# Kernel tuning notes

Measured on AMD Instinct MI355X. Metric: run time of the kernel, lower is better.

## Reference

```python
import jax, jax.numpy as jnp
import numpy as np
import math

EMBED_DIM = 1024
NUM_HEADS = 16
HEAD_DIM = EMBED_DIM // NUM_HEADS


def alibi_slopes(num_heads: int) -> np.ndarray:
    def slopes_pow2(n):
        start = 2.0 ** (-(2.0 ** (-(math.log2(n) - 3))))
        return [start * (start ** i) for i in range(n)]
    if math.log2(num_heads).is_integer():
        return np.array(slopes_pow2(num_heads), dtype=np.float32)
    closest = 2 ** math.floor(math.log2(num_heads))
    extra = slopes_pow2(2 * closest)[closest:]
    return np.array(slopes_pow2(closest) + extra[: num_heads - closest], dtype=np.float32)


def setup_inputs() -> dict:
    key = jax.random.key(0)
    ks = jax.random.split(key, 9)
    B, S, E = 2, 2048, EMBED_DIM
    scale = 1.0 / math.sqrt(E)
    x = jax.random.normal(ks[0], (B, S, E), dtype=jnp.float32)
    Wq = jax.random.normal(ks[1], (E, E), dtype=jnp.float32) * scale
    Wk = jax.random.normal(ks[2], (E, E), dtype=jnp.float32) * scale
    Wv = jax.random.normal(ks[3], (E, E), dtype=jnp.float32) * scale
    Wo = jax.random.normal(ks[4], (E, E), dtype=jnp.float32) * scale
    bq = jax.random.normal(ks[5], (E,), dtype=jnp.float32) * 0.01
    bk = jax.random.normal(ks[6], (E,), dtype=jnp.float32) * 0.01
    bv = jax.random.normal(ks[7], (E,), dtype=jnp.float32) * 0.01
    bo = jax.random.normal(ks[8], (E,), dtype=jnp.float32) * 0.01
    return {"x": x, "Wq": Wq, "bq": bq, "Wk": Wk, "bk": bk,
            "Wv": Wv, "bv": bv, "Wo": Wo, "bo": bo}


def reference(x, Wq, bq, Wk, bk, Wv, bv, Wo, bo):
    B, S, E = x.shape
    H, D = NUM_HEADS, HEAD_DIM
    # Linear layers (torch convention: y = x @ W.T + b)
    q = (x @ Wq.T + bq).reshape(B, S, H, D).transpose(0, 2, 1, 3)  # [B,H,S,D]
    k = (x @ Wk.T + bk).reshape(B, S, H, D).transpose(0, 2, 1, 3)
    v = (x @ Wv.T + bv).reshape(B, S, H, D).transpose(0, 2, 1, 3)

    # ALiBi bias: -slope_h * |i - j|
    slopes = jnp.asarray(alibi_slopes(H))                      # [H]
    pos = jnp.arange(S, dtype=jnp.float32)
    rel = jnp.abs(pos[None, :] - pos[:, None])                 # [S,S]
    bias = -slopes[:, None, None] * rel[None, :, :]            # [H,S,S]

    scores = jnp.einsum('bhqd,bhkd->bhqk', q, k) / math.sqrt(D)
    scores = scores + bias[None]
    causal = jnp.tril(jnp.ones((S, S), dtype=bool))            # keep lower triangle
    scores = jnp.where(causal[None, None], scores, -jnp.inf)
    probs = jax.nn.softmax(scores, axis=-1)
    out = jnp.einsum('bhqk,bhkd->bhqd', probs, v)              # [B,H,S,D]
    out = out.transpose(0, 2, 1, 3).reshape(B, S, E)
    return out @ Wo.T + bo
```

## Files before the change

kernel.cpp:

```cpp
#include <hip/hip_runtime.h>
#include <hip/hip_bf16.h>

typedef __bf16 bf16;
typedef __bf16 bf16x8 __attribute__((ext_vector_type(8)));
typedef float  f32x4  __attribute__((ext_vector_type(4)));

#define NEG_BIG (-1e30f)

#define AS1(p) ((const __attribute__((address_space(1))) void*)(p))
#define AS3(p) ((__attribute__((address_space(3))) void*)(p))

__device__ __forceinline__ void stage16(const void* g, void* lds_uniform_base) {
    __builtin_amdgcn_global_load_lds(AS1(g), AS3(lds_uniform_base), 16, 0, 0);
}

__device__ __forceinline__ bf16x8 cvt8(const float* __restrict__ p) {
    bf16x8 r;
#pragma unroll
    for (int i = 0; i < 8; ++i) r[i] = (bf16)p[i];
    return r;
}

__global__ __launch_bounds__(256) void conv_all(
    const float* __restrict__ x,  const float* __restrict__ wq,
    const float* __restrict__ wk, const float* __restrict__ wv,
    bf16* __restrict__ xb, bf16* __restrict__ wb)
{
    const int blk = blockIdx.x;
    const float* src; bf16* dst; size_t off;
    if (blk < 2048)      { src = x;  dst = xb;           off = (size_t)blk * 2048; }
    else if (blk < 2560) { src = wq; dst = wb;           off = (size_t)(blk - 2048) * 2048; }
    else if (blk < 3072) { src = wk; dst = wb + 1048576; off = (size_t)(blk - 2560) * 2048; }
    else                 { src = wv; dst = wb + 2097152; off = (size_t)(blk - 3072) * 2048; }
    const size_t i = off + (size_t)threadIdx.x * 8;
    *(bf16x8*)(dst + i) = cvt8(src + i);
}

__global__ __launch_bounds__(256) void qkv_gemm(
    const bf16* __restrict__ Xb, const bf16* __restrict__ Wb,
    const float* __restrict__ bq, const float* __restrict__ bk, const float* __restrict__ bv,
    bf16* __restrict__ qo, bf16* __restrict__ ko, bf16* __restrict__ vo)
{
    __shared__ alignas(16) bf16 As[128 * 32];
    __shared__ alignas(16) bf16 Bs[128 * 32];

    const int t    = threadIdx.x;
    const int lane = t & 63, w = t >> 6;
    const int quad = lane >> 4, col = lane & 15;
    const int nt = blockIdx.x;
    const int mt = blockIdx.y;
    const int region = nt >> 3;
    const int n0 = (nt & 7) * 128;
    const int m0 = mt * 128;
    const int K  = 1024;

    const bf16*  W    = Wb + (size_t)region * 1048576;
    const float* bias = region == 0 ? bq : (region == 1 ? bk : bv);
    bf16*        out  = region == 0 ? qo : (region == 1 ? ko : vo);
    const float scale = region == 0 ? 0.125f : 1.0f;

    const int wm = (w >> 1) * 64, wn = (w & 1) * 64;
    f32x4 acc[4][4] = {};

    for (int k0 = 0; k0 < K; k0 += 32) {
        __syncthreads();
#pragma unroll
        for (int i = 0; i < 2; ++i) {
            int c = i * 256 + t;
            stage16(Xb + (size_t)(m0 + (c >> 2)) * K + k0 + (c & 3) * 8,
                    As + (i * 256 + w * 64) * 8);
        }
#pragma unroll
        for (int i = 0; i < 2; ++i) {
            int c = i * 256 + t;
            stage16(W + (size_t)(n0 + (c >> 2)) * K + k0 + (c & 3) * 8,
                    Bs + (i * 256 + w * 64) * 8);
        }
        __syncthreads();

        bf16x8 a[4], b[4];
#pragma unroll
        for (int i = 0; i < 4; ++i)
            a[i] = *(const bf16x8*)(As + (wm + i * 16 + col) * 32 + quad * 8);
#pragma unroll
        for (int j = 0; j < 4; ++j)
            b[j] = *(const bf16x8*)(Bs + (wn + j * 16 + col) * 32 + quad * 8);
#pragma unroll
        for (int i = 0; i < 4; ++i)
#pragma unroll
            for (int j = 0; j < 4; ++j)
                acc[i][j] = __builtin_amdgcn_mfma_f32_16x16x32_bf16(a[i], b[j], acc[i][j], 0, 0, 0);
    }

#pragma unroll
    for (int i = 0; i < 4; ++i) {
        const int mbase = m0 + wm + i * 16 + quad * 4;
#pragma unroll
        for (int j = 0; j < 4; ++j) {
            const int n = n0 + wn + j * 16 + col;
            const float bb = bias[n];
            const int h = n >> 6, d = n & 63;
#pragma unroll
            for (int r = 0; r < 4; ++r) {
                const int m  = mbase + r;
                const int b_ = m >> 11, s = m & 2047;
                out[(((size_t)(b_ * 16 + h)) * 2048 + s) * 64 + d] =
                    (bf16)((acc[i][j][r] + bb) * scale);
            }
        }
    }
}

__global__ __launch_bounds__(256) void attn_kernel(
    const bf16* __restrict__ Q, const bf16* __restrict__ Kg,
    const bf16* __restrict__ Vg, bf16* __restrict__ O)
{
    const int t    = threadIdx.x;
    const int lane = t & 63, w = t >> 6;
    const int quad = lane >> 4, col = lane & 15;
    const int bh   = blockIdx.x & 31;
    const int pair = blockIdx.x >> 5;
    const int b  = bh >> 4, h = bh & 15;
    const float nslope = -exp2f(-0.5f * (float)(h + 1));

    const bf16* qp = Q  + (size_t)bh * 2048 * 64;
    const bf16* kp = Kg + (size_t)bh * 2048 * 64;
    const bf16* vp = Vg + (size_t)bh * 2048 * 64;

    __shared__ alignas(16) bf16 KP[4 * 32 * 136];
    __shared__ alignas(16) bf16 Vt[64 * 136];
    bf16* Ks = KP;
    bf16* Pw = KP + w * (32 * 136);

    for (int pass = 0; pass < 2; ++pass) {
        const int qt = pass == 0 ? (15 - pair) : pair;
        const int q0 = qt * 128;

        bf16x8 qa[2][2];
#pragma unroll
        for (int mi = 0; mi < 2; ++mi)
#pragma unroll
            for (int ks = 0; ks < 2; ++ks)
                qa[mi][ks] = *(const bf16x8*)(qp + (size_t)(q0 + w * 32 + mi * 16 + col) * 64
                                              + ks * 32 + quad * 8);

        float mrow[2][4], lrow[2][4];
        f32x4 of[2][4] = {};
#pragma unroll
        for (int mi = 0; mi < 2; ++mi)
#pragma unroll
            for (int r = 0; r < 4; ++r) { mrow[mi][r] = NEG_BIG; lrow[mi][r] = 0.f; }

        for (int kvt = 0; kvt <= qt; ++kvt) {
            const int kv0 = kvt * 128;

            bf16x8 kx[4], va[2], vb_[2];
#pragma unroll
            for (int i = 0; i < 4; ++i) {
                int c = i * 256 + t;
                kx[i] = *(const bf16x8*)(kp + (size_t)(kv0 + (c >> 3)) * 64 + (c & 7) * 8);
            }
#pragma unroll
            for (int i = 0; i < 2; ++i) {
                int c = i * 256 + t;
                va[i]  = *(const bf16x8*)(vp + (size_t)(kv0 + (c >> 3) * 2)     * 64 + (c & 7) * 8);
                vb_[i] = *(const bf16x8*)(vp + (size_t)(kv0 + (c >> 3) * 2 + 1) * 64 + (c & 7) * 8);
            }
            __syncthreads();
#pragma unroll
            for (int i = 0; i < 4; ++i) {
                int c = i * 256 + t;
                *(bf16x8*)(Ks + (c >> 3) * 72 + (c & 7) * 8) = kx[i];
            }
#pragma unroll
            for (int i = 0; i < 2; ++i) {
                int c = i * 256 + t;
                int kvp = c >> 3, dc = (c & 7) * 8;
#pragma unroll
                for (int e = 0; e < 8; ++e) {
                    Vt[(dc + e) * 136 + kvp * 2]     = va[i][e];
                    Vt[(dc + e) * 136 + kvp * 2 + 1] = vb_[i][e];
                }
            }
            __syncthreads();

            f32x4 sc[2][8];
#pragma unroll
            for (int nj = 0; nj < 8; ++nj) {
                bf16x8 k0f = *(const bf16x8*)(Ks + (nj * 16 + col) * 72 + quad * 8);
                bf16x8 k1f = *(const bf16x8*)(Ks + (nj * 16 + col) * 72 + 32 + quad * 8);
#pragma unroll
                for (int mi = 0; mi < 2; ++mi) {
                    f32x4 z = {};
                    z = __builtin_amdgcn_mfma_f32_16x16x32_bf16(qa[mi][0], k0f, z, 0, 0, 0);
                    z = __builtin_amdgcn_mfma_f32_16x16x32_bf16(qa[mi][1], k1f, z, 0, 0, 0);
                    sc[mi][nj] = z;
                }
            }

            const bool diag = (kvt == qt);
#pragma unroll
            for (int mi = 0; mi < 2; ++mi) {
#pragma unroll
                for (int r = 0; r < 4; ++r) {
                    const int gi = q0 + w * 32 + mi * 16 + quad * 4 + r;
                    float mx = NEG_BIG;
#pragma unroll
                    for (int nj = 0; nj < 8; ++nj) {
                        const int gj = kv0 + nj * 16 + col;
                        float val = sc[mi][nj][r] + nslope * (float)(gi - gj);
                        if (diag && gj > gi) val = NEG_BIG;
                        sc[mi][nj][r] = val;
                        mx = fmaxf(mx, val);
                    }
#pragma unroll
                    for (int off = 1; off < 16; off <<= 1)
                        mx = fmaxf(mx, __shfl_xor(mx, off, 16));
                    const float mo = mrow[mi][r];
                    const float mn = fmaxf(mo, mx);
                    const float alpha = __expf(mo - mn);
                    float rs = 0.f;
#pragma unroll
                    for (int nj = 0; nj < 8; ++nj) {
                        float p = __expf(sc[mi][nj][r] - mn);
                        sc[mi][nj][r] = p;
                        rs += p;
                    }
#pragma unroll
                    for (int off = 1; off < 16; off <<= 1)
                        rs += __shfl_xor(rs, off, 16);
                    mrow[mi][r] = mn;
                    lrow[mi][r] = lrow[mi][r] * alpha + rs;
#pragma unroll
                    for (int jd = 0; jd < 4; ++jd) of[mi][jd][r] *= alpha;
                }
            }

            __syncthreads();

#pragma unroll
            for (int mi = 0; mi < 2; ++mi)
#pragma unroll
                for (int nj = 0; nj < 8; ++nj)
#pragma unroll
                    for (int r = 0; r < 4; ++r)
                        Pw[(mi * 16 + quad * 4 + r) * 136 + nj * 16 + col] = (bf16)sc[mi][nj][r];

#pragma unroll
            for (int kk = 0; kk < 4; ++kk) {
                bf16x8 pa0 = *(const bf16x8*)(Pw + (col)      * 136 + kk * 32 + quad * 8);
                bf16x8 pa1 = *(const bf16x8*)(Pw + (16 + col) * 136 + kk * 32 + quad * 8);
#pragma unroll
                for (int jd = 0; jd < 4; ++jd) {
                    bf16x8 vbf = *(const bf16x8*)(Vt + (jd * 16 + col) * 136 + kk * 32 + quad * 8);
                    of[0][jd] = __builtin_amdgcn_mfma_f32_16x16x32_bf16(pa0, vbf, of[0][jd], 0, 0, 0);
                    of[1][jd] = __builtin_amdgcn_mfma_f32_16x16x32_bf16(pa1, vbf, of[1][jd], 0, 0, 0);
                }
            }
        }

#pragma unroll
        for (int mi = 0; mi < 2; ++mi)
#pragma unroll
            for (int r = 0; r < 4; ++r) {
                const int s = q0 + w * 32 + mi * 16 + quad * 4 + r;
                const float inv_l = 1.f / lrow[mi][r];
#pragma unroll
                for (int jd = 0; jd < 4; ++jd) {
                    const int e = h * 64 + jd * 16 + col;
                    O[((size_t)(b * 2048 + s)) * 1024 + e] = (bf16)(of[mi][jd][r] * inv_l);
                }
            }
    }
}

__global__ __launch_bounds__(256) void out_gemm(
    const bf16* __restrict__ A, const float* __restrict__ W,
    const float* __restrict__ bias, float* __restrict__ out)
{
    __shared__ alignas(16) bf16 As[128 * 32];
    __shared__ alignas(16) bf16 Bs[128 * 32];

    const int t    = threadIdx.x;
    const int lane = t & 63, w = t >> 6;
    const int quad = lane >> 4, col = lane & 15;
    const int n0 = blockIdx.x * 128;
    const int m0 = blockIdx.y * 128;
    const int K  = 1024;
    const int wm = (w >> 1) * 64, wn = (w & 1) * 64;
    const int r0 = t >> 2, c8 = (t & 3) * 8;
    f32x4 acc[4][4] = {};

    for (int k0 = 0; k0 < K; k0 += 32) {
        bf16x8 bx0 = cvt8(W + (size_t)(n0 + r0)      * K + k0 + c8);
        bf16x8 bx1 = cvt8(W + (size_t)(n0 + 64 + r0) * K + k0 + c8);
        __syncthreads();
#pragma unroll
        for (int i = 0; i < 2; ++i) {
            int c = i * 256 + t;
            stage16(A + (size_t)(m0 + (c >> 2)) * K + k0 + (c & 3) * 8,
                    As + (i * 256 + w * 64) * 8);
        }
        *(bf16x8*)(Bs + r0 * 32 + c8)        = bx0;
        *(bf16x8*)(Bs + (64 + r0) * 32 + c8) = bx1;
        __syncthreads();

        bf16x8 a[4], b[4];
#pragma unroll
        for (int i = 0; i < 4; ++i)
            a[i] = *(const bf16x8*)(As + (wm + i * 16 + col) * 32 + quad * 8);
#pragma unroll
        for (int j = 0; j < 4; ++j)
            b[j] = *(const bf16x8*)(Bs + (wn + j * 16 + col) * 32 + quad * 8);
#pragma unroll
        for (int i = 0; i < 4; ++i)
#pragma unroll
            for (int j = 0; j < 4; ++j)
                acc[i][j] = __builtin_amdgcn_mfma_f32_16x16x32_bf16(a[i], b[j], acc[i][j], 0, 0, 0);
    }

#pragma unroll
    for (int i = 0; i < 4; ++i) {
        const int mbase = m0 + wm + i * 16 + quad * 4;
#pragma unroll
        for (int j = 0; j < 4; ++j) {
            const int n = n0 + wn + j * 16 + col;
            const float bb = bias[n];
#pragma unroll
            for (int r = 0; r < 4; ++r)
                out[(size_t)(mbase + r) * 1024 + n] = acc[i][j][r] + bb;
        }
    }
}

extern "C" void kernel_launch(void* const* d_in, const int* in_sizes, int n_in,
                              void* d_out, int out_size, void* d_ws, size_t ws_size,
                              hipStream_t stream) {
    const float* x  = (const float*)d_in[0];
    const float* Wq = (const float*)d_in[1];
    const float* bq = (const float*)d_in[2];
    const float* Wk = (const float*)d_in[3];
    const float* bk = (const float*)d_in[4];
    const float* Wv = (const float*)d_in[5];
    const float* bv = (const float*)d_in[6];
    const float* Wo = (const float*)d_in[7];
    const float* bo = (const float*)d_in[8];
    float* out = (float*)d_out;

    bf16* xb  = (bf16*)d_ws;
    bf16* qws = xb  + 4194304;
    bf16* kws = qws + 4194304;
    bf16* vws = kws + 4194304;
    bf16* aws = xb;

    bf16* wb = (bf16*)d_out;

    conv_all<<<dim3(3584), 256, 0, stream>>>(x, Wq, Wk, Wv, xb, wb);
    qkv_gemm<<<dim3(24, 32), 256, 0, stream>>>(xb, wb, bq, bk, bv, qws, kws, vws);
    attn_kernel<<<dim3(256), 256, 0, stream>>>(qws, kws, vws, aws);
    out_gemm<<<dim3(8, 32), 256, 0, stream>>>(aws, Wo, bo, out);
}
```

Measured before the change: 237.4 us.

## Double-buffer K/V via async LDS loads and pre-transpose V in QKV epilogue

The QKV GEMM epilogue now writes V already transposed ([bh][d][s]) with packed 4-wide stores. It also folds log2(e) into the Q scale so the attention softmax can use exp2. The attention kernel stages K and V tiles with global_load_lds into double-buffered, XOR-swizzled LDS, prefetching the next tile while computing the current one. This removes the register round-trip, the scalar LDS transpose of V and one barrier per iteration. Row reductions use DPP instead of shuffles, and the ALiBi bias is precomputed as row and column terms; the trade-off is more LDS use and a reliance on correct async-load visibility at the barrier.

Result: faster. 216.9 us (-8.6%).

```diff
diff --git a/kernel.cpp b/kernel.cpp
--- a/kernel.cpp
+++ b/kernel.cpp
@@ -2,10 +2,12 @@
 #include <hip/hip_bf16.h>
 
 typedef __bf16 bf16;
+typedef __bf16 bf16x4 __attribute__((ext_vector_type(4)));
 typedef __bf16 bf16x8 __attribute__((ext_vector_type(8)));
 typedef float  f32x4  __attribute__((ext_vector_type(4)));
 
 #define NEG_BIG (-1e30f)
+#define LOG2E 1.44269504088896340736f
 
 #define AS1(p) ((const __attribute__((address_space(1))) void*)(p))
 #define AS3(p) ((__attribute__((address_space(3))) void*)(p))
@@ -20,6 +22,39 @@
     for (int i = 0; i < 8; ++i) r[i] = (bf16)p[i];
     return r;
 }
+
+template <int CTRL>
+__device__ __forceinline__ float dpp_max_step(float x) {
+    int v = __builtin_bit_cast(int, x);
+    int s = __builtin_amdgcn_update_dpp(v, v, CTRL, 0xF, 0xF, true);
+    return fmaxf(x, __builtin_bit_cast(float, s));
+}
+template <int CTRL>
+__device__ __forceinline__ float dpp_add_step(float x) {
+    int v = __builtin_bit_cast(int, x);
+    int s = __builtin_amdgcn_update_dpp(v, v, CTRL, 0xF, 0xF, true);
+    return x + __builtin_bit_cast(float, s);
+}
+__device__ __forceinline__ float red16_max(float x) {
+    x = dpp_max_step<0xB1>(x);
+    x = dpp_max_step<0x4E>(x);
+    x = dpp_max_step<0x141>(x);
+    x = dpp_max_step<0x140>(x);
+    return x;
+}
+__device__ __forceinline__ float red16_sum(float x) {
+    x = dpp_add_step<0xB1>(x);
+    x = dpp_add_step<0x4E>(x);
+    x = dpp_add_step<0x141>(x);
+    x = dpp_add_step<0x140>(x);
+    return x;
+}
+
+#if __has_builtin(__builtin_amdgcn_exp2f)
+#define EXP2F(x) __builtin_amdgcn_exp2f(x)
+#else
+#define EXP2F(x) exp2f(x)
+#endif
 
 __global__ __launch_bounds__(256) void conv_all(
     const float* __restrict__ x,  const float* __restrict__ wq,
@@ -56,8 +91,6 @@
 
     const bf16*  W    = Wb + (size_t)region * 1048576;
     const float* bias = region == 0 ? bq : (region == 1 ? bk : bv);
-    bf16*        out  = region == 0 ? qo : (region == 1 ? ko : vo);
-    const float scale = region == 0 ? 0.125f : 1.0f;
 
     const int wm = (w >> 1) * 64, wn = (w & 1) * 64;
     f32x4 acc[4][4] = {};
@@ -92,20 +125,40 @@
                 acc[i][j] = __builtin_amdgcn_mfma_f32_16x16x32_bf16(a[i], b[j], acc[i][j], 0, 0, 0);
     }
 
-#pragma unroll
-    for (int i = 0; i < 4; ++i) {
-        const int mbase = m0 + wm + i * 16 + quad * 4;
-#pragma unroll
-        for (int j = 0; j < 4; ++j) {
-            const int n = n0 + wn + j * 16 + col;
-            const float bb = bias[n];
-            const int h = n >> 6, d = n & 63;
-#pragma unroll
-            for (int r = 0; r < 4; ++r) {
-                const int m  = mbase + r;
-                const int b_ = m >> 11, s = m & 2047;
-                out[(((size_t)(b_ * 16 + h)) * 2048 + s) * 64 + d] =
-                    (bf16)((acc[i][j][r] + bb) * scale);
+    if (region == 2) {
+#pragma unroll
+        for (int i = 0; i < 4; ++i) {
+            const int mbase = m0 + wm + i * 16 + quad * 4;
+            const int b_ = mbase >> 11, s = mbase & 2047;
+#pragma unroll
+            for (int j = 0; j < 4; ++j) {
+                const int n = n0 + wn + j * 16 + col;
+                const float bb = bias[n];
+                const int h = n >> 6, d = n & 63;
+                bf16x4 pk;
+#pragma unroll
+                for (int r = 0; r < 4; ++r) pk[r] = (bf16)(acc[i][j][r] + bb);
+                *(bf16x4*)(vo + ((size_t)(b_ * 16 + h) * 64 + d) * 2048 + s) = pk;
+            }
+        }
+    } else {
+        bf16* out = region == 0 ? qo : ko;
+        const float scale = region == 0 ? (0.125f * LOG2E) : 1.0f;
+#pragma unroll
+        for (int i = 0; i < 4; ++i) {
+            const int mbase = m0 + wm + i * 16 + quad * 4;
+#pragma unroll
+            for (int j = 0; j < 4; ++j) {
+                const int n = n0 + wn + j * 16 + col;
+                const float bb = bias[n];
+                const int h = n >> 6, d = n & 63;
+#pragma unroll
+                for (int r = 0; r < 4; ++r) {
+                    const int m  = mbase + r;
+                    const int b_ = m >> 11, s = m & 2047;
+                    out[(((size_t)(b_ * 16 + h)) * 2048 + s) * 64 + d] =
+                        (bf16)((acc[i][j][r] + bb) * scale);
+                }
             }
         }
     }
@@ -113,7 +166,7 @@
 
 __global__ __launch_bounds__(256) void attn_kernel(
     const bf16* __restrict__ Q, const bf16* __restrict__ Kg,
-    const bf16* __restrict__ Vg, bf16* __restrict__ O)
+    const bf16* __restrict__ Vt, bf16* __restrict__ O)
 {
     const int t    = threadIdx.x;
     const int lane = t & 63, w = t >> 6;
@@ -121,16 +174,16 @@
     const int bh   = blockIdx.x & 31;
     const int pair = blockIdx.x >> 5;
     const int b  = bh >> 4, h = bh & 15;
-    const float nslope = -exp2f(-0.5f * (float)(h + 1));
-
-    const bf16* qp = Q  + (size_t)bh * 2048 * 64;
-    const bf16* kp = Kg + (size_t)bh * 2048 * 64;
-    const bf16* vp = Vg + (size_t)bh * 2048 * 64;
-
-    __shared__ alignas(16) bf16 KP[4 * 32 * 136];
-    __shared__ alignas(16) bf16 Vt[64 * 136];
-    bf16* Ks = KP;
-    bf16* Pw = KP + w * (32 * 136);
+    const float nslope = -EXP2F(-0.5f * (float)(h + 1)) * LOG2E;
+
+    const bf16* qp  = Q  + (size_t)bh * 2048 * 64;
+    const bf16* kp  = Kg + (size_t)bh * 2048 * 64;
+    const bf16* vtp = Vt + (size_t)bh * 64 * 2048;
+
+    __shared__ alignas(16) bf16 Kbuf[2][128 * 64];
+    __shared__ alignas(16) bf16 Vbuf[2][64 * 128];
+    __shared__ alignas(16) bf16 Ps[4 * 32 * 136];
+    bf16* Pw = Ps + w * (32 * 136);
 
     for (int pass = 0; pass < 2; ++pass) {
         const int qt = pass == 0 ? (15 - pair) : pair;
@@ -146,49 +199,65 @@
 
         float mrow[2][4], lrow[2][4];
         f32x4 of[2][4] = {};
-#pragma unroll
-        for (int mi = 0; mi < 2; ++mi)
-#pragma unroll
-            for (int r = 0; r < 4; ++r) { mrow[mi][r] = NEG_BIG; lrow[mi][r] = 0.f; }
+        float bi[2][4];
+        int   gi0[2];
+#pragma unroll
+        for (int mi = 0; mi < 2; ++mi) {
+            gi0[mi] = q0 + w * 32 + mi * 16 + quad * 4;
+#pragma unroll
+            for (int r = 0; r < 4; ++r) {
+                mrow[mi][r] = NEG_BIG; lrow[mi][r] = 0.f;
+                bi[mi][r] = nslope * (float)(gi0[mi] + r);
+            }
+        }
+
+        {
+#pragma unroll
+            for (int i = 0; i < 4; ++i) {
+                int c = i * 256 + t;
+                int row = c >> 3, j8 = (c & 7) ^ (row & 7);
+                stage16(kp + (size_t)row * 64 + j8 * 8, Kbuf[0] + (i * 256 + w * 64) * 8);
+            }
+#pragma unroll
+            for (int i = 0; i < 4; ++i) {
+                int c = i * 256 + t;
+                int d = c >> 4, j8 = (c & 15) ^ (d & 7);
+                stage16(vtp + (size_t)d * 2048 + j8 * 8, Vbuf[0] + (i * 256 + w * 64) * 8);
+            }
+        }
+        __syncthreads();
 
         for (int kvt = 0; kvt <= qt; ++kvt) {
             const int kv0 = kvt * 128;
-
-            bf16x8 kx[4], va[2], vb_[2];
-#pragma unroll
-            for (int i = 0; i < 4; ++i) {
-                int c = i * 256 + t;
-                kx[i] = *(const bf16x8*)(kp + (size_t)(kv0 + (c >> 3)) * 64 + (c & 7) * 8);
-            }
-#pragma unroll
-            for (int i = 0; i < 2; ++i) {
-                int c = i * 256 + t;
-                va[i]  = *(const bf16x8*)(vp + (size_t)(kv0 + (c >> 3) * 2)     * 64 + (c & 7) * 8);
-                vb_[i] = *(const bf16x8*)(vp + (size_t)(kv0 + (c >> 3) * 2 + 1) * 64 + (c & 7) * 8);
-            }
-            __syncthreads();
-#pragma unroll
-            for (int i = 0; i < 4; ++i) {
-                int c = i * 256 + t;
-                *(bf16x8*)(Ks + (c >> 3) * 72 + (c & 7) * 8) = kx[i];
-            }
-#pragma unroll
-            for (int i = 0; i < 2; ++i) {
-                int c = i * 256 + t;
-                int kvp = c >> 3, dc = (c & 7) * 8;
-#pragma unroll
-                for (int e = 0; e < 8; ++e) {
-                    Vt[(dc + e) * 136 + kvp * 2]     = va[i][e];
-                    Vt[(dc + e) * 136 + kvp * 2 + 1] = vb_[i][e];
-                }
-            }
-            __syncthreads();
+            const bf16* Kb = Kbuf[kvt & 1];
+            const bf16* Vb = Vbuf[kvt & 1];
+
+            if (kvt < qt) {
+                bf16* Kn = Kbuf[(kvt & 1) ^ 1];
+                bf16* Vn = Vbuf[(kvt & 1) ^ 1];
+                const int nv0 = kv0 + 128;
+#pragma unroll
+                for (int i = 0; i < 4; ++i) {
+                    int c = i * 256 + t;
+                    int row = c >> 3, j8 = (c & 7) ^ (row & 7);
+                    stage16(kp + (size_t)(nv0 + row) * 64 + j8 * 8, Kn + (i * 256 + w * 64) * 8);
+                }
+#pragma unroll
+                for (int i = 0; i < 4; ++i) {
+                    int c = i * 256 + t;
+                    int d = c >> 4, j8 = (c & 15) ^ (d & 7);
+                    stage16(vtp + (size_t)d * 2048 + nv0 + j8 * 8, Vn + (i * 256 + w * 64) * 8);
+                }
+            }
 
             f32x4 sc[2][8];
 #pragma unroll
             for (int nj = 0; nj < 8; ++nj) {
-                bf16x8 k0f = *(const bf16x8*)(Ks + (nj * 16 + col) * 72 + quad * 8);
-                bf16x8 k1f = *(const bf16x8*)(Ks + (nj * 16 + col) * 72 + 32 + quad * 8);
+                const int row = nj * 16 + col;
+                const bf16* kb = Kb + row * 64;
+                const int rx = row & 7;
+                bf16x8 k0f = *(const bf16x8*)(kb + (quad ^ rx) * 8);
+                bf16x8 k1f = *(const bf16x8*)(kb + ((quad + 4) ^ rx) * 8);
 #pragma unroll
                 for (int mi = 0; mi < 2; ++mi) {
                     f32x4 z = {};
@@ -199,44 +268,45 @@
             }
 
             const bool diag = (kvt == qt);
+            float bj[8];
+#pragma unroll
+            for (int nj = 0; nj < 8; ++nj)
+                bj[nj] = nslope * (float)(kv0 + nj * 16 + col);
+
 #pragma unroll
             for (int mi = 0; mi < 2; ++mi) {
 #pragma unroll
                 for (int r = 0; r < 4; ++r) {
-                    const int gi = q0 + w * 32 + mi * 16 + quad * 4 + r;
-                    float mx = NEG_BIG;
-#pragma unroll
-                    for (int nj = 0; nj < 8; ++nj) {
-                        const int gj = kv0 + nj * 16 + col;
-                        float val = sc[mi][nj][r] + nslope * (float)(gi - gj);
-                        if (diag && gj > gi) val = NEG_BIG;
-                        sc[mi][nj][r] = val;
-                        mx = fmaxf(mx, val);
+#pragma unroll
+                    for (int nj = 0; nj < 8; ++nj)
+                        sc[mi][nj][r] += bi[mi][r] - bj[nj];
+                    if (diag) {
+                        const int gi = gi0[mi] + r;
+#pragma unroll
+                        for (int nj = 0; nj < 8; ++nj)
+                            if (kv0 + nj * 16 + col > gi) sc[mi][nj][r] = NEG_BIG;
                     }
-#pragma unroll
-                    for (int off = 1; off < 16; off <<= 1)
-                        mx = fmaxf(mx, __shfl_xor(mx, off, 16));
+                    float mx = sc[mi][0][r];
+#pragma unroll
+                    for (int nj = 1; nj < 8; ++nj) mx = fmaxf(mx, sc[mi][nj][r]);
+                    mx = red16_max(mx);
                     const float mo = mrow[mi][r];
                     const float mn = fmaxf(mo, mx);
-                    const float alpha = __expf(mo - mn);
+                    const float alpha = EXP2F(mo - mn);
                     float rs = 0.f;
 #pragma unroll
                     for (int nj = 0; nj < 8; ++nj) {
-                        float p = __expf(sc[mi][nj][r] - mn);
+                        float p = EXP2F(sc[mi][nj][r] - mn);
                         sc[mi][nj][r] = p;
                         rs += p;
                     }
-#pragma unroll
-                    for (int off = 1; off < 16; off <<= 1)
-                        rs += __shfl_xor(rs, off, 16);
+                    rs = red16_sum(rs);
                     mrow[mi][r] = mn;
                     lrow[mi][r] = lrow[mi][r] * alpha + rs;
 #pragma unroll
                     for (int jd = 0; jd < 4; ++jd) of[mi][jd][r] *= alpha;
                 }
             }
-
-            __syncthreads();
 
 #pragma unroll
             for (int mi = 0; mi < 2; ++mi)
@@ -252,11 +322,14 @@
                 bf16x8 pa1 = *(const bf16x8*)(Pw + (16 + col) * 136 + kk * 32 + quad * 8);
 #pragma unroll
                 for (int jd = 0; jd < 4; ++jd) {
-                    bf16x8 vbf = *(const bf16x8*)(Vt + (jd * 16 + col) * 136 + kk * 32 + quad * 8);
+                    const int rd = jd * 16 + col;
+                    bf16x8 vbf = *(const bf16x8*)(Vb + rd * 128 + (((kk * 4 + quad) ^ (rd & 7)) * 8));
                     of[0][jd] = __builtin_amdgcn_mfma_f32_16x16x32_bf16(pa0, vbf, of[0][jd], 0, 0, 0);
                     of[1][jd] = __builtin_amdgcn_mfma_f32_16x16x32_bf16(pa1, vbf, of[1][jd], 0, 0, 0);
                 }
             }
+
+            __syncthreads();
         }
 
 #pragma unroll
```
